# Kernel tuning notes

Measured on AMD Instinct MI355X. Metric: run time of the kernel, lower is better.

The kernel has to match this reference:

```python
import jax, jax.numpy as jnp
import numpy as np

K_RATIO = 0.5  # pooling ratio k from __init__


def setup_inputs() -> dict:
    key = jax.random.key(0)
    k1, k2, k3, k4, k5 = jax.random.split(key, 5)
    N, E, D = 8192, 262144, 256
    h = jax.random.normal(k1, (N, D), dtype=jnp.float32)
    edge_index = jax.random.randint(k2, (2, E), 0, N, dtype=jnp.int64)
    edge_attr = jnp.ones((E,), dtype=jnp.float32)
    batch = jax.random.randint(k3, (N,), 0, 16, dtype=jnp.int64)
    # nn.Linear(in_dim, 1): weight [1, D] -> stored as [D] vector, bias scalar
    proj_w = jax.random.normal(k4, (D,), dtype=jnp.float32) / np.sqrt(D)
    proj_b = jax.random.normal(k5, (1,), dtype=jnp.float32)
    return {"h": h, "edge_index": edge_index, "edge_attr": edge_attr,
            "batch": batch, "proj_w": proj_w, "proj_b": proj_b}


def reference(h, edge_index, edge_attr, batch, proj_w, proj_b):
    N = batch.shape[0]
    E = edge_index.shape[1]
    # proj + squeeze + sigmoid (dropout is Identity since drop_ratio=0)
    scores = jax.nn.sigmoid(h @ proj_w + proj_b[0])  # [N]
    kN = max(2, int(K_RATIO * N))
    values, idx = jax.lax.top_k(scores, kN)  # [kN], [kN]
    # gather kept node features and scale by their scores
    new_h = h[idx, :] * values[:, None]  # [kN, D]
    # edge_attr is overwritten with ones in the original
    edge_attr_out = jnp.ones((E,), dtype=h.dtype)
    # sparse->dense adjacency (duplicate edges sum, like torch sparse to_dense)
    g = jnp.zeros((N, N), dtype=h.dtype).at[edge_index[0], edge_index[1]].add(1.0)
    # 2-hop connectivity via dense matmul, then double gather by idx
    un_g = g @ g  # [N, N]
    un_g = un_g[idx, :][:, idx]  # [kN, kN]
    new_batch = batch[idx]
    # NOTE: the torch code returns edge_index = nonzero(un_g).T, which has a
    # data-dependent shape; we return the dense pooled adjacency un_g instead
    # (edge_index is exactly its nonzero pattern).
    return new_h, un_g, edge_attr_out, new_batch, idx
```

## Files before the change

### kernel.cpp

```cpp
#include <hip/hip_runtime.h>


typedef unsigned long long u64;
typedef unsigned int u32;
typedef float f32x4 __attribute__((ext_vector_type(4)));

__device__ __forceinline__ void nt_store4(float* p, float x, float y, float z, float w) {
    f32x4 v = { x, y, z, w };
    __builtin_nontemporal_store(v, (f32x4*)p);
}

__global__ void fused_scores(const float* __restrict__ h, const float* __restrict__ w,
                             const float* __restrict__ b, u64* __restrict__ keys,
                             int* __restrict__ zerobuf, float* __restrict__ ones_out,
                             int N, int n4) {
    int g = blockIdx.x * blockDim.x + threadIdx.x;
    if (g < 2 * N) zerobuf[g] = 0;
    if (g < n4) nt_store4(ones_out + (size_t)g * 4, 1.f, 1.f, 1.f, 1.f);
    int wave = g >> 6;
    int lane = threadIdx.x & 63;
    if (wave >= N) return;
    const float4 a = ((const float4*)(h + (size_t)wave * 256))[lane];
    const float4 c = ((const float4*)w)[lane];
    float s = a.x * c.x + a.y * c.y + a.z * c.z + a.w * c.w;
    #pragma unroll
    for (int off = 32; off; off >>= 1) s += __shfl_xor(s, off);
    if (lane == 0) {
        s += b[0];
        float sc = 1.0f / (1.0f + expf(-s));
        keys[wave] = ((u64)__float_as_uint(sc) << 32) | (u32)(~wave);
    }
}

__global__ void rank_hist(const u64* __restrict__ keys, int* __restrict__ rankcnt,
                          const int* __restrict__ ei0, int* __restrict__ deg,
                          int N, int E, int nrank) {
    __shared__ u64 lk[1024];
    int b = blockIdx.x, tid = threadIdx.x;
    if (b < nrank) {
        int ngroups = N >> 8;
        int chunk = b / ngroups;
        int elg = b % ngroups;
        int base = chunk << 10;
        #pragma unroll
        for (int j = 0; j < 4; ++j) lk[tid + (j << 8)] = keys[base + tid + (j << 8)];
        __syncthreads();
        int el = (elg << 8) + tid;
        u64 mk = keys[el];
        int cnt = 0;
        #pragma unroll 16
        for (int i = 0; i < 1024; ++i) cnt += (lk[i] > mk) ? 1 : 0;
        atomicAdd(&rankcnt[el], cnt);
    } else {
        int e0 = ((b - nrank) << 10) + tid;
        #pragma unroll
        for (int j = 0; j < 4; ++j) {
            int e = e0 + (j << 8);
            if (e < E) atomicAdd(&deg[ei0[e]], 1);
        }
    }
}

__global__ void select_scan(const u64* __restrict__ keys, const int* __restrict__ rankcnt,
                            const int* __restrict__ batch, int* __restrict__ idx_list,
                            float* __restrict__ val_list, int* __restrict__ rank,
                            float* __restrict__ out_idx, float* __restrict__ out_batch,
                            const int* __restrict__ deg, int* __restrict__ offs,
                            int* __restrict__ cursor, int N, int kN) {
    __shared__ int part[1024];
    int b = blockIdx.x, t = threadIdx.x;
    int nsel = N >> 10;
    if (b < nsel) {
        int i = (b << 10) + t;
        int r = rankcnt[i];
        rank[i] = (r < kN) ? r : kN;
        if (r < kN) {
            idx_list[r] = i;
            val_list[r] = __uint_as_float((u32)(keys[i] >> 32));
            out_idx[r] = (float)i;
            out_batch[r] = (float)batch[i];
        }
    } else {
        int per = N >> 10;
        int base = t * per;
        int loc[8];
        int s = 0;
        #pragma unroll
        for (int j = 0; j < 8; ++j) { if (j < per) { loc[j] = s; s += deg[base + j]; } }
        part[t] = s;
        __syncthreads();
        for (int d = 1; d < 1024; d <<= 1) {
            int v = (t >= d) ? part[t - d] : 0;
            __syncthreads();
            part[t] += v;
            __syncthreads();
        }
        int excl = (t == 0) ? 0 : part[t - 1];
        #pragma unroll
        for (int j = 0; j < 8; ++j) {
            if (j < per) { int o = excl + loc[j]; offs[base + j] = o; cursor[base + j] = o; }
        }
        if (t == 1023) offs[N] = part[1023];
    }
}

__global__ void newh_scatter(const float* __restrict__ h, const int* __restrict__ idx_list,
                             const float* __restrict__ val_list, float* __restrict__ out_newh,
                             const int* __restrict__ ei0, const int* __restrict__ ei1,
                             int* __restrict__ cursor, const int* __restrict__ offs,
                             const int* __restrict__ deg, const int* __restrict__ rank,
                             int2* __restrict__ desc, int* __restrict__ nbrrank,
                             int kN, int E) {
    int b = blockIdx.x, tid = threadIdx.x;
    int nnewh = kN >> 2;
    if (b < nnewh) {
        int wave = (b << 2) + (tid >> 6);
        int lane = tid & 63;
        int i = idx_list[wave];
        float v = val_list[wave];
        float4 a = ((const float4*)(h + (size_t)i * 256))[lane];
        nt_store4(out_newh + (size_t)wave * 256 + lane * 4,
                  a.x * v, a.y * v, a.z * v, a.w * v);
    } else {
        int e = ((b - nnewh) << 8) + tid;
        if (e < E) {
            int u = ei0[e], v = ei1[e];
            int p = atomicAdd(&cursor[u], 1);
            desc[p] = make_int2(offs[v], deg[v]);
            nbrrank[p] = rank[v];
        }
    }
}

__global__ void paths_row_kernel(const int* __restrict__ idx_list, const int* __restrict__ offs,
                                 const int2* __restrict__ desc, const int* __restrict__ nbrrank,
                                 float* __restrict__ ung, int kN) {
    extern __shared__ float row[];
    int* toff = (int*)(row + kN);
    int* tlen = toff + 256;
    int tid = threadIdx.x;
    float4* row4 = (float4*)row;
    float4 z4 = make_float4(0.f, 0.f, 0.f, 0.f);
    for (int i = tid; i < (kN >> 2); i += 256) row4[i] = z4;
    __syncthreads();
    int u = idx_list[blockIdx.x];
    int s0 = offs[u], s1 = offs[u + 1];
    int nf = s1 - s0;
    int wid = tid >> 6;
    int lane = tid & 63;
    for (int fb = 0; fb < nf; fb += 256) {
        int nt = min(256, nf - fb);
        if (tid < nt) {
            int2 dd = desc[s0 + fb + tid];
            toff[tid] = dd.x; tlen[tid] = dd.y;
        }
        __syncthreads();
        for (int f0 = wid; f0 < nt; f0 += 256) {
            int va[16];
            #pragma unroll
            for (int k = 0; k < 16; ++k) {
                int f = f0 + (k << 2);
                va[k] = kN;
                if (f < nt) {
                    int t0 = toff[f], L = tlen[f];
                    if (lane < L) va[k] = nbrrank[t0 + lane];
                }
            }
            #pragma unroll
            for (int k = 0; k < 16; ++k)
                if (va[k] < kN) atomicAdd(&row[va[k]], 1.0f);
            #pragma unroll
            for (int k = 0; k < 16; ++k) {
                int f = f0 + (k << 2);
                if (f < nt) {
                    int t0 = toff[f], L = tlen[f];
                    for (int q = lane + 64; q < L; q += 64) {
                        int r = nbrrank[t0 + q];
                        if (r < kN) atomicAdd(&row[r], 1.0f);
                    }
                }
            }
        }
        __syncthreads();
    }
    float* dst = ung + (size_t)blockIdx.x * kN;
    for (int i = tid; i < (kN >> 2); i += 256) {
        float4 v = row4[i];
        nt_store4(dst + (size_t)i * 4, v.x, v.y, v.z, v.w);
    }
}

extern "C" void kernel_launch(void* const* d_in, const int* in_sizes, int n_in,
                              void* d_out, int out_size, void* d_ws, size_t ws_size,
                              hipStream_t stream) {
    const float* h = (const float*)d_in[0];
    const int* ei = (const int*)d_in[1];
    const int* batch = (const int*)d_in[3];
    const float* pw = (const float*)d_in[4];
    const float* pb = (const float*)d_in[5];

    int N = in_sizes[3];
    int E = in_sizes[1] / 2;
    int kN = N / 2;
    if (kN < 2) kN = 2;

    float* out = (float*)d_out;
    float* out_newh = out;
    float* out_ung = out_newh + (size_t)kN * 256;
    float* out_ea = out_ung + (size_t)kN * kN;
    float* out_nb = out_ea + E;
    float* out_idx = out_nb + kN;

    char* ws = (char*)d_ws;
    u64* keys    = (u64*)(ws + 0);
    int* rankcnt = (int*)(ws + 65536);
    int* deg     = (int*)(ws + 98304);
    int* idx_list= (int*)(ws + 131072);
    float* vals  = (float*)(ws + 147456);
    int* rank    = (int*)(ws + 163840);
    int* offs    = (int*)(ws + 196608);
    int* cursor  = (int*)(ws + 229632);
    int2* desc   = (int2*)(ws + 262400);
    int* nbrrank = (int*)(ws + 2359552);

    fused_scores<<<(N * 64 + 255) / 256, 256, 0, stream>>>(h, pw, pb, keys, rankcnt,
                                                           out_ea, N, E / 4);
    int nrank = (N >> 10) * (N >> 8);
    int nhist = (E + 1023) / 1024;
    rank_hist<<<nrank + nhist, 256, 0, stream>>>(keys, rankcnt, ei, deg, N, E, nrank);
    select_scan<<<(N >> 10) + 1, 1024, 0, stream>>>(keys, rankcnt, batch, idx_list, vals,
                                                    rank, out_idx, out_nb, deg, offs,
                                                    cursor, N, kN);
    newh_scatter<<<(kN >> 2) + (E >> 8), 256, 0, stream>>>(h, idx_list, vals, out_newh,
                                                           ei, ei + E, cursor, offs, deg,
                                                           rank, desc, nbrrank, kN, E);
    paths_row_kernel<<<kN, 256, (size_t)kN * 4 + 2048, stream>>>(idx_list, offs, desc,
                                                                 nbrrank, out_ung, kN);
}
```

Baseline: 83.38 us.

## Pack CSR entries into 32-bit words and pad cursor atomics

The per-edge CSR entry is reduced from an int2 descriptor plus a separate rank array to one 32-bit word holding the neighbour id in the high 16 bits and its rank in the low 16 bits. The second-hop offsets and lengths are now read from offs in the row kernel. Each per-node cursor is spaced 16 ints apart so atomics on different nodes do not share cache lines. The row kernel's work split changes so each wave takes 16 consecutive first-hop neighbours per 64-entry chunk. This cuts scatter write traffic and gather read bytes, at the cost of extra offs lookups, a larger cursor footprint in the workspace, and a reliance on N and kN fitting in 16 bits.

```diff
diff --git a/kernel.cpp b/kernel.cpp
--- a/kernel.cpp
+++ b/kernel.cpp
@@ -98,7 +98,11 @@
         int excl = (t == 0) ? 0 : part[t - 1];
         #pragma unroll
         for (int j = 0; j < 8; ++j) {
-            if (j < per) { int o = excl + loc[j]; offs[base + j] = o; cursor[base + j] = o; }
+            if (j < per) {
+                int o = excl + loc[j];
+                offs[base + j] = o;
+                cursor[(base + j) << 4] = o;
+            }
         }
         if (t == 1023) offs[N] = part[1023];
     }
@@ -107,10 +111,8 @@
 __global__ void newh_scatter(const float* __restrict__ h, const int* __restrict__ idx_list,
                              const float* __restrict__ val_list, float* __restrict__ out_newh,
                              const int* __restrict__ ei0, const int* __restrict__ ei1,
-                             int* __restrict__ cursor, const int* __restrict__ offs,
-                             const int* __restrict__ deg, const int* __restrict__ rank,
-                             int2* __restrict__ desc, int* __restrict__ nbrrank,
-                             int kN, int E) {
+                             int* __restrict__ cursor, const int* __restrict__ rank,
+                             u32* __restrict__ pk, int kN, int E) {
     int b = blockIdx.x, tid = threadIdx.x;
     int nnewh = kN >> 2;
     if (b < nnewh) {
@@ -125,16 +127,14 @@
         int e = ((b - nnewh) << 8) + tid;
         if (e < E) {
             int u = ei0[e], v = ei1[e];
-            int p = atomicAdd(&cursor[u], 1);
-            desc[p] = make_int2(offs[v], deg[v]);
-            nbrrank[p] = rank[v];
+            int p = atomicAdd(&cursor[u << 4], 1);
+            pk[p] = ((u32)v << 16) | (u32)rank[v];
         }
     }
 }
 
 __global__ void paths_row_kernel(const int* __restrict__ idx_list, const int* __restrict__ offs,
-                                 const int2* __restrict__ desc, const int* __restrict__ nbrrank,
-                                 float* __restrict__ ung, int kN) {
+                                 const u32* __restrict__ pk, float* __restrict__ ung, int kN) {
     extern __shared__ float row[];
     int* toff = (int*)(row + kN);
     int* tlen = toff + 256;
@@ -148,35 +148,39 @@
     int nf = s1 - s0;
     int wid = tid >> 6;
     int lane = tid & 63;
+    u32 ukN = (u32)kN;
     for (int fb = 0; fb < nf; fb += 256) {
         int nt = min(256, nf - fb);
         if (tid < nt) {
-            int2 dd = desc[s0 + fb + tid];
-            toff[tid] = dd.x; tlen[tid] = dd.y;
-        }
-        __syncthreads();
-        for (int f0 = wid; f0 < nt; f0 += 256) {
-            int va[16];
+            u32 val = pk[s0 + fb + tid];
+            int v = (int)(val >> 16);
+            int a = offs[v];
+            toff[tid] = a;
+            tlen[tid] = offs[v + 1] - a;
+        }
+        __syncthreads();
+        for (int base = 0; base < nt; base += 64) {
+            u32 va[16];
             #pragma unroll
             for (int k = 0; k < 16; ++k) {
-                int f = f0 + (k << 2);
-                va[k] = kN;
+                int f = base + (wid << 4) + k;
+                va[k] = ukN;
                 if (f < nt) {
                     int t0 = toff[f], L = tlen[f];
-                    if (lane < L) va[k] = nbrrank[t0 + lane];
+                    if (lane < L) va[k] = pk[t0 + lane] & 0xFFFFu;
                 }
             }
             #pragma unroll
             for (int k = 0; k < 16; ++k)
-                if (va[k] < kN) atomicAdd(&row[va[k]], 1.0f);
+                if (va[k] < ukN) atomicAdd(&row[va[k]], 1.0f);
             #pragma unroll
             for (int k = 0; k < 16; ++k) {
-                int f = f0 + (k << 2);
+                int f = base + (wid << 4) + k;
                 if (f < nt) {
                     int t0 = toff[f], L = tlen[f];
                     for (int q = lane + 64; q < L; q += 64) {
-                        int r = nbrrank[t0 + q];
-                        if (r < kN) atomicAdd(&row[r], 1.0f);
+                        u32 r = pk[t0 + q] & 0xFFFFu;
+                        if (r < ukN) atomicAdd(&row[r], 1.0f);
                     }
                 }
             }
@@ -220,8 +224,7 @@
     int* rank    = (int*)(ws + 163840);
     int* offs    = (int*)(ws + 196608);
     int* cursor  = (int*)(ws + 229632);
-    int2* desc   = (int2*)(ws + 262400);
-    int* nbrrank = (int*)(ws + 2359552);
+    u32* pk      = (u32*)(ws + 753920);
 
     fused_scores<<<(N * 64 + 255) / 256, 256, 0, stream>>>(h, pw, pb, keys, rankcnt,
                                                            out_ea, N, E / 4);
@@ -232,8 +235,8 @@
                                                     rank, out_idx, out_nb, deg, offs,
                                                     cursor, N, kN);
     newh_scatter<<<(kN >> 2) + (E >> 8), 256, 0, stream>>>(h, idx_list, vals, out_newh,
-                                                           ei, ei + E, cursor, offs, deg,
-                                                           rank, desc, nbrrank, kN, E);
-    paths_row_kernel<<<kN, 256, (size_t)kN * 4 + 2048, stream>>>(idx_list, offs, desc,
-                                                                 nbrrank, out_ung, kN);
-}
+                                                           ei, ei + E, cursor, rank,
+                                                           pk, kN, E);
+    paths_row_kernel<<<kN, 256, (size_t)kN * 4 + 2048, stream>>>(idx_list, offs, pk,
+                                                                 out_ung, kN);
+}
```

After: 85.03 us. About the same (+2.0%).
